# Optimization experiments

Measured on AMD Instinct MI355X. Metric: run time of the kernel, lower is better.

## Reference

```python
import jax, jax.numpy as jnp
import numpy as np

# ---- constants (match init_kwargs) ----
H = 16            # bit depth of location codes
TP = 8            # number of parallel location dims
N = 1 << H        # location magnitude bound
N_K = 2
N_C = 2 * H * N_K + 1   # 65 candidate locations per token
T = 512           # T_train
N_TTNBR = 64
K_VOCAB = 128
S = N_TTNBR + K_VOCAB   # 192
D = 256           # dim_eu
TEMP = 0.05


def cos_similarity(c1, c2):
    """CritiGraph frexp-based cosine: sign product * (1 - bitlength(|a|^|b| + 1)/h)."""
    sg = (2 * (c1 >= 0).astype(jnp.int32) - 1) * (2 * (c2 >= 0).astype(jnp.int32) - 1)
    x = jnp.abs(c1) ^ jnp.abs(c2)
    _, e = jnp.frexp((x + 1).astype(jnp.float32))  # exponent == bit_length(x+1)
    return sg.astype(jnp.float32) * (1.0 - e.astype(jnp.float32) / H)


def setup_inputs() -> dict:
    key = jax.random.key(0)
    ks = jax.random.split(key, 8)
    loc = lambda k, shape: jax.random.randint(k, shape, 1 - N, N, dtype=jnp.int32)
    return {
        "cur_tar": jax.random.randint(ks[0], (T,), 0, K_VOCAB, dtype=jnp.int32),
        "cnc_loc": loc(ks[1], (T, N_C, TP)),
        "sta_loc": loc(ks[2], (T, TP)),
        "ttn_loc": loc(ks[3], (T, N_TTNBR, TP)),
        "voc_loc": loc(ks[4], (T, K_VOCAB, TP)),
        "sta_emb": 0.1 * jax.random.normal(ks[5], (T, D), dtype=jnp.float32),
        "ttn_emb": 0.1 * jax.random.normal(ks[6], (T, N_TTNBR, D), dtype=jnp.float32),
        "voc_emb": 0.1 * jax.random.normal(ks[7], (T, K_VOCAB, D), dtype=jnp.float32),
    }


def reference(cur_tar, cnc_loc, sta_loc, ttn_loc, voc_loc, sta_emb, ttn_emb, voc_emb):
    # positives = dynamic neighbors ++ sampled vocab
    pos_loc = jnp.concatenate([ttn_loc, voc_loc], axis=1)      # (T, S, TP) int32
    pos_emb = jnp.concatenate([ttn_emb, voc_emb], axis=1)      # (T, S, D)

    # Euclidean-space logits
    eu_val = 20.0 * TEMP * jnp.einsum('td,tsd->ts', sta_emb, pos_emb)  # (T, S)

    # CT-space similarities
    cos_sp = cos_similarity(sta_loc[:, None, :], pos_loc)      # (T, S, TP)
    cos_sum = cos_sp.sum(axis=-1)                              # (T, S)
    # candidate location swapped into each track d (ct_val_triton math)
    cos_cp = cos_similarity(cnc_loc[:, None, :, :], pos_loc[:, :, None, :])  # (T, S, N_C, TP)
    ct_val = (cos_sum[:, :, None, None] - cos_sp[:, :, None, :] + cos_cp) / TP \
             * (20.0 * TEMP)                                   # (T, S, N_C, TP)

    # KL(eu || ct) over the dynamic neighbors
    logits_ct_dyn = ct_val[:, :N_TTNBR]                        # (T, Nn, N_C, TP)
    logits_eu_dyn = eu_val[:, :N_TTNBR]                        # (T, Nn)
    p_eu = jax.nn.softmax(logits_eu_dyn, axis=1)
    lp_eu = jax.nn.log_softmax(logits_eu_dyn, axis=1)
    lp_ct = jax.nn.log_softmax(logits_ct_dyn, axis=1)
    loss_dyn_dyn = (p_eu[:, :, None, None] * (lp_eu[:, :, None, None] - lp_ct)).sum(axis=1)  # (T, N_C, TP)

    # cross-entropy over the sampled vocab
    logits_ct_sta = ct_val[:, N_TTNBR:] / TEMP                 # (T, K, N_C, TP)
    logits_flat = logits_ct_sta.reshape(T, K_VOCAB, N_C * TP)
    log_probs = jax.nn.log_softmax(logits_flat, axis=1)        # (T, K, N_C*TP)
    idx = jnp.broadcast_to(cur_tar[:, None, None].astype(jnp.int32), (T, 1, N_C * TP))
    target_lp = jnp.take_along_axis(log_probs, idx, axis=1)[:, 0, :]  # (T, N_C*TP)
    loss_dyn_sta = -target_lp.reshape(T, N_C, TP)              # (T, N_C, TP)

    return loss_dyn_dyn, loss_dyn_sta
```

## Files before the change

kernel.cpp:

```cpp
#include <hip/hip_runtime.h>


#define Tn   512
#define NC   65
#define TPd  8
#define NTn  64
#define KV   128
#define Sn   192
#define Dn   256
#define OUT1 (Tn * NC * TPd)

#define LOG2E 1.44269504088896340736f
#define LN2   0.69314718055994530942f
#define ADYN (0.125f * LOG2E * 0.0625f)
#define ASTA (2.5f  * LOG2E * 0.0625f)
#define ARAW 0.0625f

__device__ __forceinline__ float exp2_fast(float x) {
#if __has_builtin(__builtin_amdgcn_exp2f)
    return __builtin_amdgcn_exp2f(x);
#else
    return exp2f(x);
#endif
}
__device__ __forceinline__ float asf(int v) { return __int_as_float(v); }
__device__ __forceinline__ int   asi(float v) { return __float_as_int(v); }

__device__ __forceinline__ int pack15(int v) {
    int a = (v < 0) ? -v : v;
    return (a << 15) | (int)(((unsigned)v) >> 31);
}
__device__ __forceinline__ float cos15(int y, float A) {
    int   x = y + 0x8000;
    float c = fmaf((float)__clz(x), A, -A);
    return asf(asi(c) ^ (y << 31));
}

__device__ __forceinline__ int eidx(int s, int p) {
    return ((s >> 1) * TPd + p) * 2 + (s & 1);
}

__global__ __launch_bounds__(512, 4) void critigraph_kernel(
    const int*   __restrict__ cur_tar,
    const int*   __restrict__ cnc_loc,
    const int*   __restrict__ sta_loc,
    const int*   __restrict__ ttn_loc,
    const int*   __restrict__ voc_loc,
    const float* __restrict__ sta_emb,
    const float* __restrict__ ttn_emb,
    float*       __restrict__ out)
{
    __shared__ int2  s_dyn2[NTn * TPd];
    __shared__ int2  s_sta2[KV * TPd];
    __shared__ float s_b2d[NTn * TPd];
    __shared__ int   s_cnc[NC * TPd];
    __shared__ int   s_staloc[TPd];
    __shared__ float s_csum[Sn];
    __shared__ float s_eu[NTn];
    __shared__ float s_peu[NTn];
    __shared__ float s_dotbase[TPd];
    __shared__ float s_kl;

    const int t   = blockIdx.x;
    const int tid = threadIdx.x;
    const int tar = cur_tar[t];

    if (tid < TPd) s_staloc[tid] = pack15(sta_loc[t * TPd + tid]);
    for (int i = tid; i < NC * TPd; i += 512)
        s_cnc[i] = pack15(cnc_loc[t * NC * TPd + i]);
    __syncthreads();

    const int mysta = s_staloc[tid & 7];
    float mysp[3];
    #pragma unroll
    for (int k = 0; k < 3; ++k) {
        int i = tid + 512 * k;
        int s = i >> 3;
        int p = i & 7;
        int v = (s < NTn) ? ttn_loc[t * NTn * TPd + i]
                          : voc_loc[t * KV * TPd + (i - NTn * TPd)];
        int packed = pack15(v);
        float c = cos15(packed ^ mysta, ARAW);
        mysp[k] = c;
        if (s < NTn) s_dyn2[eidx(s, p)].x = packed;
        else         s_sta2[eidx(s - NTn, p)].x = packed;
        float v8 = c;
        v8 += __shfl_xor(v8, 1);
        v8 += __shfl_xor(v8, 2);
        v8 += __shfl_xor(v8, 4);
        if (p == 0) s_csum[s] = v8;
    }
    {
        const int r = tid >> 3, q = tid & 7;
        const float4* A = (const float4*)(sta_emb + (size_t)t * Dn);
        const float4* B = (const float4*)(ttn_emb + ((size_t)t * NTn + r) * Dn);
        float acc = 0.f;
        #pragma unroll
        for (int k = 0; k < 8; ++k) {
            float4 a = A[k * 8 + q];
            float4 b = B[k * 8 + q];
            acc += a.x * b.x + a.y * b.y + a.z * b.z + a.w * b.w;
        }
        acc += __shfl_xor(acc, 1);
        acc += __shfl_xor(acc, 2);
        acc += __shfl_xor(acc, 4);
        if (q == 0) s_eu[r] = acc;
    }
    __syncthreads();

    #pragma unroll
    for (int k = 0; k < 3; ++k) {
        int i = tid + 512 * k;
        int s = i >> 3;
        int p = i & 7;
        if (s < NTn) {
            float b2 = (s_csum[s] - mysp[k]) * (0.125f * LOG2E);
            int   e  = eidx(s, p);
            s_dyn2[e].y = asi(exp2_fast(b2));
            s_b2d[e]    = b2;
        } else {
            float b2 = (s_csum[s] - mysp[k]) * (2.5f * LOG2E);
            s_sta2[eidx(s - NTn, p)].y = asi(exp2_fast(b2));
        }
    }
    if (tid < 64) {
        float e  = s_eu[tid];
        float mx = e;
        #pragma unroll
        for (int m = 1; m < 64; m <<= 1) mx = fmaxf(mx, __shfl_xor(mx, m));
        float ex = __expf(e - mx);
        float z  = ex;
        #pragma unroll
        for (int m = 1; m < 64; m <<= 1) z += __shfl_xor(z, m);
        float pe = ex / z;
        s_peu[tid] = pe;
        float kls = pe * ((e - mx) - __logf(z));
        #pragma unroll
        for (int m = 1; m < 64; m <<= 1) kls += __shfl_xor(kls, m);
        if (tid == 0) s_kl = kls;
    }
    __syncthreads();

    {
        int i = tid;
        int s = (((i >> 4) << 1) | (i & 1));
        int Eb = s_dyn2[i].y;
        int Pb = asi(s_peu[s]);
        s_dyn2[i].y = (int)((((unsigned)Eb + 0x8000u) & 0xFFFF0000u) |
                            (((unsigned)Pb + 0x8000u) >> 16));
    }
    if (tid < 64) {
        int g = tid & 7, j = tid >> 3;
        float a = 0.f;
        #pragma unroll
        for (int k = 0; k < 8; ++k) {
            int s = 8 * j + k;
            a = fmaf(s_peu[s], s_b2d[eidx(s, g)], a);
        }
        #pragma unroll
        for (int m = 8; m < 64; m <<= 1) a += __shfl_xor(a, m);
        if (tid < TPd) s_dotbase[g] = a;
    }
    __syncthreads();

    const int   p    = tid & 7;
    const int   acnc = s_cnc[tid];
    const float kl   = s_kl;
    const float dtb  = s_dotbase[p];
    const int4* dyn4 = (const int4*)s_dyn2;
    const int4* sta4 = (const int4*)s_sta2;

    float sum = 0.f, dot = 0.f;
    #pragma unroll 8
    for (int j = 0; j < NTn / 2; ++j) {
        int4 q = dyn4[j * TPd + p];
        {
            int   y  = q.x ^ acnc;
            float cc = cos15(y, ADYN);
            float E  = asf(q.y & (int)0xFFFF0000);
            float pe = asf(q.y << 16);
            sum = fmaf(E, exp2_fast(cc), sum);
            dot = fmaf(pe, cc, dot);
        }
        {
            int   y  = q.z ^ acnc;
            float cc = cos15(y, ADYN);
            float E  = asf(q.w & (int)0xFFFF0000);
            float pe = asf(q.w << 16);
            sum = fmaf(E, exp2_fast(cc), sum);
            dot = fmaf(pe, cc, dot);
        }
    }
    float s2 = 0.f;
    #pragma unroll 8
    for (int j = 0; j < KV / 2; ++j) {
        int4 q = sta4[j * TPd + p];
        s2 = fmaf(asf(q.y), exp2_fast(cos15(q.x ^ acnc, ASTA)), s2);
        s2 = fmaf(asf(q.w), exp2_fast(cos15(q.z ^ acnc, ASTA)), s2);
    }
    {
        int2  tq  = s_sta2[eidx(tar, p)];
        float b2t = __log2f(asf(tq.y));
        float cct = cos15(tq.x ^ acnc, ASTA);
        float* od = out + (size_t)t * NC * TPd;
        float* os = out + OUT1 + (size_t)t * NC * TPd;
        od[tid] = kl + LN2 * (__log2f(sum) - (dtb + dot));
        os[tid] = LN2 * (__log2f(s2) - (b2t + cct));
    }

    {
        const int w    = tid >> 6;
        const int lane = tid & 63;
        const int acw  = s_cnc[512 + w];
        float sumd, dotd, sums;
        {
            int2  q  = s_dyn2[eidx(lane, w)];
            int   y  = q.x ^ acw;
            float cc = cos15(y, ADYN);
            sumd = asf(q.y & (int)0xFFFF0000) * exp2_fast(cc);
            dotd = asf(q.y << 16) * cc;
        }
        {
            int2 q0 = s_sta2[eidx(lane, w)];
            int2 q1 = s_sta2[eidx(lane + 64, w)];
            sums = asf(q0.y) * exp2_fast(cos15(q0.x ^ acw, ASTA))
                 + asf(q1.y) * exp2_fast(cos15(q1.x ^ acw, ASTA));
        }
        #pragma unroll
        for (int m = 1; m < 64; m <<= 1) {
            sumd += __shfl_xor(sumd, m);
            dotd += __shfl_xor(dotd, m);
            sums += __shfl_xor(sums, m);
        }
        if (lane == 0) {
            int2  tq  = s_sta2[eidx(tar, w)];
            float b2t = __log2f(asf(tq.y));
            float cct = cos15(tq.x ^ acw, ASTA);
            out[(size_t)t * NC * TPd + 512 + w] =
                kl + LN2 * (__log2f(sumd) - (s_dotbase[w] + dotd));
            out[OUT1 + (size_t)t * NC * TPd + 512 + w] =
                LN2 * (__log2f(sums) - (b2t + cct));
        }
    }
}

extern "C" void kernel_launch(void* const* d_in, const int* in_sizes, int n_in,
                              void* d_out, int out_size, void* d_ws, size_t ws_size,
                              hipStream_t stream) {
    (void)in_sizes; (void)n_in; (void)d_ws; (void)ws_size; (void)out_size;
    const int*   cur_tar = (const int*)  d_in[0];
    const int*   cnc_loc = (const int*)  d_in[1];
    const int*   sta_loc = (const int*)  d_in[2];
    const int*   ttn_loc = (const int*)  d_in[3];
    const int*   voc_loc = (const int*)  d_in[4];
    const float* sta_emb = (const float*)d_in[5];
    const float* ttn_emb = (const float*)d_in[6];
    critigraph_kernel<<<Tn, 512, 0, stream>>>(cur_tar, cnc_loc, sta_loc, ttn_loc,
                                              voc_loc, sta_emb, ttn_emb, (float*)d_out);
}
```

Measured before the change: 143.0 us.

## Split kernel into prep pass writing workspace and main pass over two half-blocks

The single 512-thread kernel becomes two launches. A 256-thread prep kernel packs location codes, biases, softmax weights and the KL term into a per-token blob in workspace. A main kernel with two 256-thread blocks per token reloads that blob into shared memory and computes half of the candidate outputs each, with the tail candidates handled by one half using 32-lane reductions. The aim is more, smaller blocks for better occupancy and scheduling, at the cost of an extra launch and a global-memory round trip of about 15 KB per token.

```diff
diff --git a/kernel.cpp b/kernel.cpp
--- a/kernel.cpp
+++ b/kernel.cpp
@@ -6,9 +6,11 @@
 #define TPd  8
 #define NTn  64
 #define KV   128
-#define Sn   192
 #define Dn   256
 #define OUT1 (Tn * NC * TPd)
+#define WSTRIDE 4096
+#define BLOBI   3712
+#define BLOB4   928
 
 #define LOG2E 1.44269504088896340736f
 #define LN2   0.69314718055994530942f
@@ -35,12 +37,11 @@
     float c = fmaf((float)__clz(x), A, -A);
     return asf(asi(c) ^ (y << 31));
 }
-
 __device__ __forceinline__ int eidx(int s, int p) {
     return ((s >> 1) * TPd + p) * 2 + (s & 1);
 }
 
-__global__ __launch_bounds__(512, 4) void critigraph_kernel(
+__global__ __launch_bounds__(256, 4) void crit_prep(
     const int*   __restrict__ cur_tar,
     const int*   __restrict__ cnc_loc,
     const int*   __restrict__ sta_loc,
@@ -48,42 +49,42 @@
     const int*   __restrict__ voc_loc,
     const float* __restrict__ sta_emb,
     const float* __restrict__ ttn_emb,
-    float*       __restrict__ out)
+    int*         __restrict__ ws)
 {
-    __shared__ int2  s_dyn2[NTn * TPd];
-    __shared__ int2  s_sta2[KV * TPd];
+    __shared__ int4  blob4[BLOB4];
+    int*   blob = (int*)blob4;
+    int2*  dynT = (int2*)blob;
+    int2*  staT = (int2*)(blob + 1024);
+    int*   cncT = blob + 3072;
+    float* dotb = (float*)(blob + 3600);
     __shared__ float s_b2d[NTn * TPd];
-    __shared__ int   s_cnc[NC * TPd];
-    __shared__ int   s_staloc[TPd];
-    __shared__ float s_csum[Sn];
+    __shared__ float s_csum[192];
     __shared__ float s_eu[NTn];
     __shared__ float s_peu[NTn];
-    __shared__ float s_dotbase[TPd];
-    __shared__ float s_kl;
+    __shared__ int   s_staloc[TPd];
 
     const int t   = blockIdx.x;
     const int tid = threadIdx.x;
-    const int tar = cur_tar[t];
 
     if (tid < TPd) s_staloc[tid] = pack15(sta_loc[t * TPd + tid]);
-    for (int i = tid; i < NC * TPd; i += 512)
-        s_cnc[i] = pack15(cnc_loc[t * NC * TPd + i]);
+    if (tid == 0)  blob[3609] = cur_tar[t];
+    for (int i = tid; i < NC * TPd; i += 256)
+        cncT[i] = pack15(cnc_loc[t * NC * TPd + i]);
     __syncthreads();
 
     const int mysta = s_staloc[tid & 7];
-    float mysp[3];
+    float mysp[6];
     #pragma unroll
-    for (int k = 0; k < 3; ++k) {
-        int i = tid + 512 * k;
-        int s = i >> 3;
-        int p = i & 7;
+    for (int k = 0; k < 6; ++k) {
+        int i = tid + 256 * k;
+        int s = i >> 3, p = i & 7;
         int v = (s < NTn) ? ttn_loc[t * NTn * TPd + i]
                           : voc_loc[t * KV * TPd + (i - NTn * TPd)];
         int packed = pack15(v);
         float c = cos15(packed ^ mysta, ARAW);
         mysp[k] = c;
-        if (s < NTn) s_dyn2[eidx(s, p)].x = packed;
-        else         s_sta2[eidx(s - NTn, p)].x = packed;
+        if (s < NTn) dynT[eidx(s, p)].x = packed;
+        else         staT[eidx(s - NTn, p)].x = packed;
         float v8 = c;
         v8 += __shfl_xor(v8, 1);
         v8 += __shfl_xor(v8, 2);
@@ -91,36 +92,34 @@
         if (p == 0) s_csum[s] = v8;
     }
     {
-        const int r = tid >> 3, q = tid & 7;
+        const int r = tid >> 2, q = tid & 3;
         const float4* A = (const float4*)(sta_emb + (size_t)t * Dn);
         const float4* B = (const float4*)(ttn_emb + ((size_t)t * NTn + r) * Dn);
         float acc = 0.f;
         #pragma unroll
-        for (int k = 0; k < 8; ++k) {
-            float4 a = A[k * 8 + q];
-            float4 b = B[k * 8 + q];
+        for (int k = 0; k < 16; ++k) {
+            float4 a = A[k * 4 + q];
+            float4 b = B[k * 4 + q];
             acc += a.x * b.x + a.y * b.y + a.z * b.z + a.w * b.w;
         }
         acc += __shfl_xor(acc, 1);
         acc += __shfl_xor(acc, 2);
-        acc += __shfl_xor(acc, 4);
         if (q == 0) s_eu[r] = acc;
     }
     __syncthreads();
 
     #pragma unroll
-    for (int k = 0; k < 3; ++k) {
-        int i = tid + 512 * k;
-        int s = i >> 3;
-        int p = i & 7;
+    for (int k = 0; k < 6; ++k) {
+        int i = tid + 256 * k;
+        int s = i >> 3, p = i & 7;
         if (s < NTn) {
             float b2 = (s_csum[s] - mysp[k]) * (0.125f * LOG2E);
             int   e  = eidx(s, p);
-            s_dyn2[e].y = asi(exp2_fast(b2));
-            s_b2d[e]    = b2;
+            dynT[e].y = asi(exp2_fast(b2));
+            s_b2d[e]  = b2;
         } else {
             float b2 = (s_csum[s] - mysp[k]) * (2.5f * LOG2E);
-            s_sta2[eidx(s - NTn, p)].y = asi(exp2_fast(b2));
+            staT[eidx(s - NTn, p)].y = asi(exp2_fast(b2));
         }
     }
     if (tid < 64) {
@@ -137,17 +136,18 @@
         float kls = pe * ((e - mx) - __logf(z));
         #pragma unroll
         for (int m = 1; m < 64; m <<= 1) kls += __shfl_xor(kls, m);
-        if (tid == 0) s_kl = kls;
-    }
-    __syncthreads();
-
-    {
-        int i = tid;
+        if (tid == 0) blob[3608] = asi(kls);
+    }
+    __syncthreads();
+
+    #pragma unroll
+    for (int k = 0; k < 2; ++k) {
+        int i = tid + 256 * k;
         int s = (((i >> 4) << 1) | (i & 1));
-        int Eb = s_dyn2[i].y;
+        int Eb = dynT[i].y;
         int Pb = asi(s_peu[s]);
-        s_dyn2[i].y = (int)((((unsigned)Eb + 0x8000u) & 0xFFFF0000u) |
-                            (((unsigned)Pb + 0x8000u) >> 16));
+        dynT[i].y = (int)((((unsigned)Eb + 0x8000u) & 0xFFFF0000u) |
+                          (((unsigned)Pb + 0x8000u) >> 16));
     }
     if (tid < 64) {
         int g = tid & 7, j = tid >> 3;
@@ -159,16 +159,41 @@
         }
         #pragma unroll
         for (int m = 8; m < 64; m <<= 1) a += __shfl_xor(a, m);
-        if (tid < TPd) s_dotbase[g] = a;
-    }
-    __syncthreads();
+        if (tid < TPd) dotb[g] = a;
+    }
+    __syncthreads();
+
+    int4* dst = (int4*)(ws + (size_t)t * WSTRIDE);
+    for (int i = tid; i < BLOB4; i += 256) dst[i] = blob4[i];
+}
+
+__global__ __launch_bounds__(256, 4) void crit_main(
+    const int* __restrict__ ws,
+    float*     __restrict__ out)
+{
+    __shared__ int4 blob4[BLOB4];
+    int* blob = (int*)blob4;
+
+    const int bx  = blockIdx.x;
+    const int t   = bx >> 1;
+    const int h   = bx & 1;
+    const int tid = threadIdx.x;
+
+    const int4* src = (const int4*)(ws + (size_t)t * WSTRIDE);
+    for (int i = tid; i < BLOB4; i += 256) blob4[i] = src[i];
+    __syncthreads();
+
+    const int4*  dyn4 = blob4;
+    const int4*  sta4 = blob4 + 256;
+    const int2*  staT = (const int2*)(blob + 1024);
+    const int*   cncT = blob + 3072;
+    const float* dotb = (const float*)(blob + 3600);
+    const float  kl   = asf(blob[3608]);
+    const int    tar  = blob[3609];
 
     const int   p    = tid & 7;
-    const int   acnc = s_cnc[tid];
-    const float kl   = s_kl;
-    const float dtb  = s_dotbase[p];
-    const int4* dyn4 = (const int4*)s_dyn2;
-    const int4* sta4 = (const int4*)s_sta2;
+    const int   acnc = cncT[h * 256 + tid];
+    const float dtb  = dotb[p];
 
     float sum = 0.f, dot = 0.f;
     #pragma unroll 8
@@ -177,18 +202,14 @@
         {
             int   y  = q.x ^ acnc;
             float cc = cos15(y, ADYN);
-            float E  = asf(q.y & (int)0xFFFF0000);
-            float pe = asf(q.y << 16);
-            sum = fmaf(E, exp2_fast(cc), sum);
-            dot = fmaf(pe, cc, dot);
+            sum = fmaf(asf(q.y & (int)0xFFFF0000), exp2_fast(cc), sum);
+            dot = fmaf(asf(q.y << 16), cc, dot);
         }
         {
             int   y  = q.z ^ acnc;
             float cc = cos15(y, ADYN);
-            float E  = asf(q.w & (int)0xFFFF0000);
-            float pe = asf(q.w << 16);
-            sum = fmaf(E, exp2_fast(cc), sum);
-            dot = fmaf(pe, cc, dot);
+            sum = fmaf(asf(q.w & (int)0xFFFF0000), exp2_fast(cc), sum);
+            dot = fmaf(asf(q.w << 16), cc, dot);
         }
     }
     float s2 = 0.f;
@@ -199,46 +220,50 @@
         s2 = fmaf(asf(q.w), exp2_fast(cos15(q.z ^ acnc, ASTA)), s2);
     }
     {
-        int2  tq  = s_sta2[eidx(tar, p)];
+        int2  tq  = staT[eidx(tar, p)];
         float b2t = __log2f(asf(tq.y));
         float cct = cos15(tq.x ^ acnc, ASTA);
         float* od = out + (size_t)t * NC * TPd;
         float* os = out + OUT1 + (size_t)t * NC * TPd;
-        od[tid] = kl + LN2 * (__log2f(sum) - (dtb + dot));
-        os[tid] = LN2 * (__log2f(s2) - (b2t + cct));
-    }
-
-    {
+        od[h * 256 + tid] = kl + LN2 * (__log2f(sum) - (dtb + dot));
+        os[h * 256 + tid] = LN2 * (__log2f(s2) - (b2t + cct));
+    }
+
+    if (h == 1) {
         const int w    = tid >> 6;
         const int lane = tid & 63;
-        const int acw  = s_cnc[512 + w];
-        float sumd, dotd, sums;
-        {
-            int2  q  = s_dyn2[eidx(lane, w)];
+        const int half = lane >> 5;
+        const int sub  = lane & 31;
+        const int pt   = 2 * w + half;
+        const int acw  = cncT[512 + pt];
+        const int2* dynT = (const int2*)blob;
+        float sumd = 0.f, dotd = 0.f, sums = 0.f;
+        #pragma unroll
+        for (int k = 0; k < 2; ++k) {
+            int2  q  = dynT[eidx(sub + 32 * k, pt)];
             int   y  = q.x ^ acw;
             float cc = cos15(y, ADYN);
-            sumd = asf(q.y & (int)0xFFFF0000) * exp2_fast(cc);
-            dotd = asf(q.y << 16) * cc;
-        }
-        {
-            int2 q0 = s_sta2[eidx(lane, w)];
-            int2 q1 = s_sta2[eidx(lane + 64, w)];
-            sums = asf(q0.y) * exp2_fast(cos15(q0.x ^ acw, ASTA))
-                 + asf(q1.y) * exp2_fast(cos15(q1.x ^ acw, ASTA));
-        }
-        #pragma unroll
-        for (int m = 1; m < 64; m <<= 1) {
+            sumd = fmaf(asf(q.y & (int)0xFFFF0000), exp2_fast(cc), sumd);
+            dotd = fmaf(asf(q.y << 16), cc, dotd);
+        }
+        #pragma unroll
+        for (int k = 0; k < 4; ++k) {
+            int2 q = staT[eidx(sub + 32 * k, pt)];
+            sums = fmaf(asf(q.y), exp2_fast(cos15(q.x ^ acw, ASTA)), sums);
+        }
+        #pragma unroll
+        for (int m = 1; m < 32; m <<= 1) {
             sumd += __shfl_xor(sumd, m);
             dotd += __shfl_xor(dotd, m);
             sums += __shfl_xor(sums, m);
         }
-        if (lane == 0) {
-            int2  tq  = s_sta2[eidx(tar, w)];
+        if (sub == 0) {
+            int2  tq  = staT[eidx(tar, pt)];
             float b2t = __log2f(asf(tq.y));
             float cct = cos15(tq.x ^ acw, ASTA);
-            out[(size_t)t * NC * TPd + 512 + w] =
-                kl + LN2 * (__log2f(sumd) - (s_dotbase[w] + dotd));
-            out[OUT1 + (size_t)t * NC * TPd + 512 + w] =
+            out[(size_t)t * NC * TPd + 512 + pt] =
+                kl + LN2 * (__log2f(sumd) - (dotb[pt] + dotd));
+            out[OUT1 + (size_t)t * NC * TPd + 512 + pt] =
                 LN2 * (__log2f(sums) - (b2t + cct));
         }
     }
@@ -247,7 +272,7 @@
 extern "C" void kernel_launch(void* const* d_in, const int* in_sizes, int n_in,
                               void* d_out, int out_size, void* d_ws, size_t ws_size,
                               hipStream_t stream) {
-    (void)in_sizes; (void)n_in; (void)d_ws; (void)ws_size; (void)out_size;
+    (void)in_sizes; (void)n_in; (void)ws_size; (void)out_size;
     const int*   cur_tar = (const int*)  d_in[0];
     const int*   cnc_loc = (const int*)  d_in[1];
     const int*   sta_loc = (const int*)  d_in[2];
@@ -255,6 +280,8 @@
     const int*   voc_loc = (const int*)  d_in[4];
     const float* sta_emb = (const float*)d_in[5];
     const float* ttn_emb = (const float*)d_in[6];
-    critigraph_kernel<<<Tn, 512, 0, stream>>>(cur_tar, cnc_loc, sta_loc, ttn_loc,
-                                              voc_loc, sta_emb, ttn_emb, (float*)d_out);
-}
+    int* ws = (int*)d_ws;
+    crit_prep<<<Tn, 256, 0, stream>>>(cur_tar, cnc_loc, sta_loc, ttn_loc,
+                                      voc_loc, sta_emb, ttn_emb, ws);
+    crit_main<<<Tn * 2, 256, 0, stream>>>(ws, (float*)d_out);
+}
```

After: 153.5 us. 7.3% more time.

## Replace per-candidate brute-force sums with bucketed prefix pyramid over location bits

Applied to the files above, without the earlier changes.

Positive locations are radix-bucketed by their top 6 packed bits via a shared-memory histogram and scatter, and a per-track binary pyramid of summed exp weights and softmax probabilities is built. Each candidate then reads the cosine contribution for entries that differ in a high bit from precomputed level constants, and only walks its own bucket explicitly. This replaces the O(S) per-candidate loop with roughly O(levels + bucket size). It adds atomics, several extra barriers and data-dependent loop lengths, which can diverge within a wavefront.

```diff
diff --git a/kernel.cpp b/kernel.cpp
--- a/kernel.cpp
+++ b/kernel.cpp
@@ -6,7 +6,6 @@
 #define TPd  8
 #define NTn  64
 #define KV   128
-#define Sn   192
 #define Dn   256
 #define OUT1 (Tn * NC * TPd)
 
@@ -15,6 +14,10 @@
 #define ADYN (0.125f * LOG2E * 0.0625f)
 #define ASTA (2.5f  * LOG2E * 0.0625f)
 #define ARAW 0.0625f
+
+#define PYR_P 378
+#define OFF_P 126
+#define OFF_S 252
 
 __device__ __forceinline__ float exp2_fast(float x) {
 #if __has_builtin(__builtin_amdgcn_exp2f)
@@ -25,19 +28,14 @@
 }
 __device__ __forceinline__ float asf(int v) { return __int_as_float(v); }
 __device__ __forceinline__ int   asi(float v) { return __float_as_int(v); }
-
 __device__ __forceinline__ int pack15(int v) {
     int a = (v < 0) ? -v : v;
     return (a << 15) | (int)(((unsigned)v) >> 31);
 }
 __device__ __forceinline__ float cos15(int y, float A) {
-    int   x = y + 0x8000;
+    int   x = (int)((unsigned)y + 0x8000u);
     float c = fmaf((float)__clz(x), A, -A);
     return asf(asi(c) ^ (y << 31));
-}
-
-__device__ __forceinline__ int eidx(int s, int p) {
-    return ((s >> 1) * TPd + p) * 2 + (s & 1);
 }
 
 __global__ __launch_bounds__(512, 4) void critigraph_kernel(
@@ -50,57 +48,106 @@
     const float* __restrict__ ttn_emb,
     float*       __restrict__ out)
 {
-    __shared__ int2  s_dyn2[NTn * TPd];
-    __shared__ int2  s_sta2[KV * TPd];
-    __shared__ float s_b2d[NTn * TPd];
-    __shared__ int   s_cnc[NC * TPd];
-    __shared__ int   s_staloc[TPd];
-    __shared__ float s_csum[Sn];
-    __shared__ float s_eu[NTn];
-    __shared__ float s_peu[NTn];
-    __shared__ float s_dotbase[TPd];
-    __shared__ float s_kl;
+    __shared__ float2 s_pyr[TPd * PYR_P];
+    __shared__ int2   s_dynS[NTn * TPd];
+    __shared__ int2   s_staS[KV * TPd];
+    __shared__ int    s_hist[16 * 64];
+    __shared__ int    s_starts[16 * 65];
+    __shared__ int    s_cnc[NC * TPd];
+    __shared__ float  s_b2d[NTn * TPd];
+    __shared__ float  s_peu[NTn];
+    __shared__ float  s_eu[NTn];
+    __shared__ float  s_tarE[TPd];
+    __shared__ int    s_tarK[TPd];
+    __shared__ float  s_dotb[TPd];
+    __shared__ float  s_kl;
 
     const int t   = blockIdx.x;
     const int tid = threadIdx.x;
+    const int p   = tid & 7;
     const int tar = cur_tar[t];
 
-    if (tid < TPd) s_staloc[tid] = pack15(sta_loc[t * TPd + tid]);
-    for (int i = tid; i < NC * TPd; i += 512)
-        s_cnc[i] = pack15(cnc_loc[t * NC * TPd + i]);
-    __syncthreads();
-
-    const int mysta = s_staloc[tid & 7];
-    float mysp[3];
+    s_hist[tid] = 0;
+    s_hist[tid + 512] = 0;
+    s_cnc[tid] = pack15(cnc_loc[t * NC * TPd + tid]);
+    if (tid < 8) s_cnc[512 + tid] = pack15(cnc_loc[t * NC * TPd + 512 + tid]);
+    const int mysta = pack15(sta_loc[t * TPd + p]);
+    __syncthreads();
+
+    int   keyv[3];
+    float Ev[3];
     #pragma unroll
     for (int k = 0; k < 3; ++k) {
         int i = tid + 512 * k;
         int s = i >> 3;
-        int p = i & 7;
         int v = (s < NTn) ? ttn_loc[t * NTn * TPd + i]
                           : voc_loc[t * KV * TPd + (i - NTn * TPd)];
         int packed = pack15(v);
         float c = cos15(packed ^ mysta, ARAW);
-        mysp[k] = c;
-        if (s < NTn) s_dyn2[eidx(s, p)].x = packed;
-        else         s_sta2[eidx(s - NTn, p)].x = packed;
         float v8 = c;
         v8 += __shfl_xor(v8, 1);
         v8 += __shfl_xor(v8, 2);
         v8 += __shfl_xor(v8, 4);
-        if (p == 0) s_csum[s] = v8;
-    }
+        if (s < NTn) {
+            float b2 = (v8 - c) * (0.125f * LOG2E);
+            s_b2d[i] = b2;
+            Ev[k]    = exp2_fast(b2);
+            keyv[k]  = packed | (s << 1);
+            atomicAdd(&s_hist[p * 64 + ((packed >> 25) & 63)], 1);
+        } else {
+            float b2 = (v8 - c) * (2.5f * LOG2E);
+            Ev[k]    = exp2_fast(b2);
+            keyv[k]  = packed;
+            atomicAdd(&s_hist[(8 + p) * 64 + ((packed >> 25) & 63)], 1);
+            if (s - NTn == tar) { s_tarK[p] = packed; s_tarE[p] = Ev[k]; }
+        }
+    }
+    __syncthreads();
+
+    {
+        const int lane = tid & 63;
+        #pragma unroll
+        for (int rnd = 0; rnd < 2; ++rnd) {
+            int seg = (tid >> 6) + rnd * 8;
+            int v   = s_hist[seg * 64 + lane];
+            int inc = v;
+            #pragma unroll
+            for (int off = 1; off < 64; off <<= 1) {
+                int u = __shfl_up(inc, off);
+                if (lane >= off) inc += u;
+            }
+            int base = (seg < 8) ? (seg * 64) : ((seg - 8) * 128);
+            int excl = base + inc - v;
+            s_starts[seg * 65 + lane] = excl;
+            if (lane == 63) s_starts[seg * 65 + 64] = base + inc;
+            s_hist[seg * 64 + lane] = excl;
+        }
+    }
+    __syncthreads();
+
     {
         const int r = tid >> 3, q = tid & 7;
-        const float4* A = (const float4*)(sta_emb + (size_t)t * Dn);
-        const float4* B = (const float4*)(ttn_emb + ((size_t)t * NTn + r) * Dn);
+        const float4* A4 = (const float4*)(sta_emb + (size_t)t * Dn);
+        const float4* B4 = (const float4*)(ttn_emb + ((size_t)t * NTn + r) * Dn);
+        float4 av[8], bv[8];
+        #pragma unroll
+        for (int k = 0; k < 8; ++k) { av[k] = A4[k * 8 + q]; bv[k] = B4[k * 8 + q]; }
+
+        int bk = (keyv[0] >> 25) & 63;
+        int ix = atomicAdd(&s_hist[p * 64 + bk], 1);
+        s_dynS[ix] = make_int2(keyv[0], asi(Ev[0]));
+        bk = (keyv[1] >> 25) & 63;
+        ix = atomicAdd(&s_hist[(8 + p) * 64 + bk], 1);
+        s_staS[ix] = make_int2(keyv[1], asi(Ev[1]));
+        bk = (keyv[2] >> 25) & 63;
+        ix = atomicAdd(&s_hist[(8 + p) * 64 + bk], 1);
+        s_staS[ix] = make_int2(keyv[2], asi(Ev[2]));
+
         float acc = 0.f;
         #pragma unroll
-        for (int k = 0; k < 8; ++k) {
-            float4 a = A[k * 8 + q];
-            float4 b = B[k * 8 + q];
-            acc += a.x * b.x + a.y * b.y + a.z * b.z + a.w * b.w;
-        }
+        for (int k = 0; k < 8; ++k)
+            acc += av[k].x * bv[k].x + av[k].y * bv[k].y
+                 + av[k].z * bv[k].z + av[k].w * bv[k].w;
         acc += __shfl_xor(acc, 1);
         acc += __shfl_xor(acc, 2);
         acc += __shfl_xor(acc, 4);
@@ -108,21 +155,6 @@
     }
     __syncthreads();
 
-    #pragma unroll
-    for (int k = 0; k < 3; ++k) {
-        int i = tid + 512 * k;
-        int s = i >> 3;
-        int p = i & 7;
-        if (s < NTn) {
-            float b2 = (s_csum[s] - mysp[k]) * (0.125f * LOG2E);
-            int   e  = eidx(s, p);
-            s_dyn2[e].y = asi(exp2_fast(b2));
-            s_b2d[e]    = b2;
-        } else {
-            float b2 = (s_csum[s] - mysp[k]) * (2.5f * LOG2E);
-            s_sta2[eidx(s - NTn, p)].y = asi(exp2_fast(b2));
-        }
-    }
     if (tid < 64) {
         float e  = s_eu[tid];
         float mx = e;
@@ -138,108 +170,117 @@
         #pragma unroll
         for (int m = 1; m < 64; m <<= 1) kls += __shfl_xor(kls, m);
         if (tid == 0) s_kl = kls;
-    }
-    __syncthreads();
-
-    {
-        int i = tid;
-        int s = (((i >> 4) << 1) | (i & 1));
-        int Eb = s_dyn2[i].y;
-        int Pb = asi(s_peu[s]);
-        s_dyn2[i].y = (int)((((unsigned)Eb + 0x8000u) & 0xFFFF0000u) |
-                            (((unsigned)Pb + 0x8000u) >> 16));
-    }
-    if (tid < 64) {
         int g = tid & 7, j = tid >> 3;
         float a = 0.f;
         #pragma unroll
         for (int k = 0; k < 8; ++k) {
             int s = 8 * j + k;
-            a = fmaf(s_peu[s], s_b2d[eidx(s, g)], a);
+            a = fmaf(s_peu[s], s_b2d[s * TPd + g], a);
         }
         #pragma unroll
         for (int m = 8; m < 64; m <<= 1) a += __shfl_xor(a, m);
-        if (tid < TPd) s_dotbase[g] = a;
-    }
-    __syncthreads();
-
-    const int   p    = tid & 7;
-    const int   acnc = s_cnc[tid];
-    const float kl   = s_kl;
-    const float dtb  = s_dotbase[p];
-    const int4* dyn4 = (const int4*)s_dyn2;
-    const int4* sta4 = (const int4*)s_sta2;
-
-    float sum = 0.f, dot = 0.f;
-    #pragma unroll 8
-    for (int j = 0; j < NTn / 2; ++j) {
-        int4 q = dyn4[j * TPd + p];
+        if (tid < TPd) s_dotb[g] = a;
+    }
+    __syncthreads();
+
+    {
+        const int bk = tid >> 3;
+        int st = s_starts[p * 65 + bk], en = s_starts[p * 65 + bk + 1];
+        float2 E2 = make_float2(0.f, 0.f), P2 = make_float2(0.f, 0.f);
+        for (int i = st; i < en; ++i) {
+            int2  q  = s_dynS[i];
+            float e  = asf(q.y);
+            float pe = s_peu[(q.x >> 1) & 63];
+            if (q.x & 1) { E2.y += e; P2.y += pe; } else { E2.x += e; P2.x += pe; }
+        }
+        s_pyr[p * PYR_P + 62 + bk]         = E2;
+        s_pyr[p * PYR_P + OFF_P + 62 + bk] = P2;
+        st = s_starts[(8 + p) * 65 + bk]; en = s_starts[(8 + p) * 65 + bk + 1];
+        float2 S2 = make_float2(0.f, 0.f);
+        for (int i = st; i < en; ++i) {
+            int2 q = s_staS[i];
+            if (q.x & 1) S2.y += asf(q.y); else S2.x += asf(q.y);
+        }
+        s_pyr[p * PYR_P + OFF_S + 62 + bk] = S2;
+    }
+
+    for (int L = 5; L >= 1; --L) {
+        __syncthreads();
+        const int cnt = 24 << L;
+        const int cb  = (2 << L) - 2;
+        const int pb  = (1 << L) - 2;
+        for (int j = tid; j < cnt; j += 512) {
+            int n  = j & ((1 << L) - 1);
+            int g  = j >> L;
+            int a  = g % 3;
+            int pp = g / 3;
+            int base = pp * PYR_P + a * 126;
+            float2 c0 = s_pyr[base + cb + 2 * n];
+            float2 c1 = s_pyr[base + cb + 2 * n + 1];
+            s_pyr[base + pb + n] = make_float2(c0.x + c1.x, c0.y + c1.y);
+        }
+    }
+    __syncthreads();
+
+    auto pair_eval = [&](int ac, int pp, float& outd, float& outs) {
+        const float2* pyrp = s_pyr + pp * PYR_P;
+        const int b0 = ac & 1;
+        float sum, dot = 0.f, s2;
         {
-            int   y  = q.x ^ acnc;
-            float cc = cos15(y, ADYN);
-            float E  = asf(q.y & (int)0xFFFF0000);
-            float pe = asf(q.y << 16);
-            sum = fmaf(E, exp2_fast(cc), sum);
-            dot = fmaf(pe, cc, dot);
-        }
+            int idx = ((ac >> 30) & 1) ^ 1;
+            float2 dE = pyrp[idx], sE = pyrp[idx + OFF_S];
+            sum = dE.x + dE.y;
+            s2  = sE.x + sE.y;
+        }
+#define LVL(L, CD_, TDP_, TDM_, TSP_, TSM_) { \
+        int idx = ((((ac >> (31 - (L))) & ((1 << (L)) - 1)) ^ 1) + ((1 << (L)) - 2)); \
+        float2 dE = pyrp[idx]; float2 dP = pyrp[idx + OFF_P]; float2 sE = pyrp[idx + OFF_S]; \
+        float Em = b0 ? dE.y : dE.x, En = b0 ? dE.x : dE.y; \
+        float Pm = b0 ? dP.y : dP.x, Pn = b0 ? dP.x : dP.y; \
+        float Sm = b0 ? sE.y : sE.x, Sn = b0 ? sE.x : sE.y; \
+        sum = fmaf(TDP_, Em, fmaf(TDM_, En, sum)); \
+        dot = fmaf(CD_, Pm - Pn, dot); \
+        s2  = fmaf(TSP_, Sm, fmaf(TSM_, Sn, s2)); }
+        LVL(2, 0.0112710550f, 1.00784308f, 0.99221794f, 1.16911840f, 0.85534531f)
+        LVL(3, 0.0225421100f, 1.01574770f, 0.98449643f, 1.36683784f, 0.73161561f)
+        LVL(4, 0.0338131650f, 1.02371431f, 0.97683501f, 1.59799517f, 0.62578409f)
+        LVL(5, 0.0450842200f, 1.03174341f, 0.96923323f, 1.86824557f, 0.53526138f)
+        LVL(6, 0.0563552750f, 1.03983561f, 0.96169061f, 2.18420029f, 0.45783352f)
+#undef LVL
+        const int bk = (ac >> 25) & 63;
         {
-            int   y  = q.z ^ acnc;
-            float cc = cos15(y, ADYN);
-            float E  = asf(q.w & (int)0xFFFF0000);
-            float pe = asf(q.w << 16);
-            sum = fmaf(E, exp2_fast(cc), sum);
-            dot = fmaf(pe, cc, dot);
-        }
-    }
-    float s2 = 0.f;
-    #pragma unroll 8
-    for (int j = 0; j < KV / 2; ++j) {
-        int4 q = sta4[j * TPd + p];
-        s2 = fmaf(asf(q.y), exp2_fast(cos15(q.x ^ acnc, ASTA)), s2);
-        s2 = fmaf(asf(q.w), exp2_fast(cos15(q.z ^ acnc, ASTA)), s2);
-    }
+            int st = s_starts[pp * 65 + bk], en = s_starts[pp * 65 + bk + 1];
+            for (int i = st; i < en; ++i) {
+                int2  q  = s_dynS[i];
+                int   y  = q.x ^ ac;
+                float cc = cos15(y, ADYN);
+                sum = fmaf(asf(q.y), exp2_fast(cc), sum);
+                dot = fmaf(s_peu[(y >> 1) & 63], cc, dot);
+            }
+        }
+        {
+            int st = s_starts[(8 + pp) * 65 + bk], en = s_starts[(8 + pp) * 65 + bk + 1];
+            for (int i = st; i < en; ++i) {
+                int2 q = s_staS[i];
+                s2 = fmaf(asf(q.y), exp2_fast(cos15(q.x ^ ac, ASTA)), s2);
+            }
+        }
+        float b2t = __log2f(s_tarE[pp]);
+        float cct = cos15(s_tarK[pp] ^ ac, ASTA);
+        outd = s_kl + LN2 * (__log2f(sum) - (s_dotb[pp] + dot));
+        outs = LN2 * (__log2f(s2) - (b2t + cct));
+    };
+
     {
-        int2  tq  = s_sta2[eidx(tar, p)];
-        float b2t = __log2f(asf(tq.y));
-        float cct = cos15(tq.x ^ acnc, ASTA);
-        float* od = out + (size_t)t * NC * TPd;
-        float* os = out + OUT1 + (size_t)t * NC * TPd;
-        od[tid] = kl + LN2 * (__log2f(sum) - (dtb + dot));
-        os[tid] = LN2 * (__log2f(s2) - (b2t + cct));
-    }
-
-    {
-        const int w    = tid >> 6;
-        const int lane = tid & 63;
-        const int acw  = s_cnc[512 + w];
-        float sumd, dotd, sums;
-        {
-            int2  q  = s_dyn2[eidx(lane, w)];
-            int   y  = q.x ^ acw;
-            float cc = cos15(y, ADYN);
-            sumd = asf(q.y & (int)0xFFFF0000) * exp2_fast(cc);
-            dotd = asf(q.y << 16) * cc;
-        }
-        {
-            int2 q0 = s_sta2[eidx(lane, w)];
-            int2 q1 = s_sta2[eidx(lane + 64, w)];
-            sums = asf(q0.y) * exp2_fast(cos15(q0.x ^ acw, ASTA))
-                 + asf(q1.y) * exp2_fast(cos15(q1.x ^ acw, ASTA));
-        }
-        #pragma unroll
-        for (int m = 1; m < 64; m <<= 1) {
-            sumd += __shfl_xor(sumd, m);
-            dotd += __shfl_xor(dotd, m);
-            sums += __shfl_xor(sums, m);
-        }
-        if (lane == 0) {
-            int2  tq  = s_sta2[eidx(tar, w)];
-            float b2t = __log2f(asf(tq.y));
-            float cct = cos15(tq.x ^ acw, ASTA);
-            out[(size_t)t * NC * TPd + 512 + w] =
-                kl + LN2 * (__log2f(sumd) - (s_dotbase[w] + dotd));
-            out[OUT1 + (size_t)t * NC * TPd + 512 + w] =
-                LN2 * (__log2f(sums) - (b2t + cct));
+        float od, os;
+        pair_eval(s_cnc[tid], p, od, os);
+        out[(size_t)t * NC * TPd + tid]        = od;
+        out[OUT1 + (size_t)t * NC * TPd + tid] = os;
+        if (tid < 8) {
+            float od2, os2;
+            pair_eval(s_cnc[512 + tid], tid, od2, os2);
+            out[(size_t)t * NC * TPd + 512 + tid]        = od2;
+            out[OUT1 + (size_t)t * NC * TPd + 512 + tid] = os2;
         }
     }
 }
```

Measured after the change: 130.4 us. 1.1x faster.
